# Performance work log

Hardware: AMD Instinct MI355X
Metric: run time of the kernel (lower is better)

## Reference

```python
import jax, jax.numpy as jnp
import numpy as np

SCALE = 1.0  # alpha / rank = 32 / 32


def setup_inputs() -> dict:
    key = jax.random.key(0)
    k_x, k_w, k_b, k_a, k_bb = jax.random.split(key, 5)
    B, S, D = 4, 4096, 3072
    depth, rank = 4, 32
    x = jax.random.normal(k_x, (B, S, D), dtype=jnp.float32)
    W = jax.random.normal(k_w, (D, D), dtype=jnp.float32) * (1.0 / np.sqrt(D))
    b = jax.random.normal(k_b, (D,), dtype=jnp.float32) * 0.02
    lora_A = jax.random.normal(k_a, (depth, rank, D), dtype=jnp.float32) * (1.0 / np.sqrt(D))
    lora_B = jax.random.normal(k_bb, (depth, D, rank), dtype=jnp.float32) * 0.02
    return {"x": x, "W": W, "b": b, "lora_A": lora_A, "lora_B": lora_B}


def reference(x, W, b, lora_A, lora_B):
    # base: y = x @ W.T + b
    base_out = jnp.einsum('bsi,oi->bso', x, W) + b
    # stacked LoRA: sum_d (x @ A_d.T @ B_d.T); dropout=0 -> identity
    # down-project to rank per depth: [B,S,depth,rank]
    z = jnp.einsum('bsi,dri->bsdr', x, lora_A)
    lora_out = jnp.einsum('bsdr,dor->bso', z, lora_B)
    return base_out + lora_out * SCALE
```

## Files before the change

### kernel.cpp

```cpp
#include <hip/hip_runtime.h>
#include <hip/hip_bf16.h>


typedef unsigned short ushort_t;
typedef short bf16x8 __attribute__((ext_vector_type(8)));
typedef float floatx4 __attribute__((ext_vector_type(4)));
typedef unsigned short ushortx4 __attribute__((ext_vector_type(4)));
typedef unsigned short ushortx8 __attribute__((ext_vector_type(8)));

__device__ __forceinline__ ushort_t f2bf(float f) {
    __hip_bfloat16 h = __float2bfloat16(f);
    return *(ushort_t*)&h;
}

__device__ __forceinline__ void async_load16(const void* g, void* l) {
    __builtin_amdgcn_global_load_lds(
        (const __attribute__((address_space(1))) void*)g,
        (__attribute__((address_space(3))) void*)l,
        16, 0, 0);
}

#define MFMA16(a, b, c) __builtin_amdgcn_mfma_f32_16x16x32_bf16(a, b, c, 0, 0, 0)

__global__ __launch_bounds__(256)
void cvt_kernel(const float* __restrict__ in, ushort_t* __restrict__ out, int n8) {
    int i = blockIdx.x * 256 + threadIdx.x;
    if (i < n8) {
        const float4 v0 = ((const float4*)in)[2 * i];
        const float4 v1 = ((const float4*)in)[2 * i + 1];
        ushortx8 o = { f2bf(v0.x), f2bf(v0.y), f2bf(v0.z), f2bf(v0.w),
                       f2bf(v1.x), f2bf(v1.y), f2bf(v1.z), f2bf(v1.w) };
        ((ushortx8*)out)[i] = o;
    }
}

__global__ __launch_bounds__(256)
void transpose_lora_kernel(const float* __restrict__ lb,
                           const float* __restrict__ la,
                           ushort_t* __restrict__ outB,
                           ushort_t* __restrict__ outA) {
    int bid = blockIdx.x;
    if (bid < 1536) {
        int idx = bid * 256 + threadIdx.x;
        int n = idx >> 7;
        int j = idx & 127;
        int d = j >> 5, r = j & 31;
        outB[idx] = f2bf(lb[(size_t)d * (3072 * 32) + (size_t)n * 32 + r]);
    } else {
        int idx = (bid - 1536) * 256 + threadIdx.x;
        int kk = idx >> 7;
        int j  = idx & 127;
        outA[idx] = f2bf(la[(size_t)j * 3072 + kk]);
    }
}

template <int KT, bool OUT_F32, bool ADD_MAT>
__global__ __launch_bounds__(256)
void gemm_bt_kernel(const ushort_t* __restrict__ A, int lda,
                    const ushort_t* __restrict__ B, int ldb,
                    const float* __restrict__ Cadd,
                    const float* __restrict__ bias,
                    void* __restrict__ Cv, int ldc)
{
    __shared__ ushort_t As[128 * 32];
    __shared__ ushort_t Bs[128 * 32];

    const int t    = threadIdx.x;
    const int lane = t & 63;
    const int wave = t >> 6;
    const int wr   = wave >> 1, wc = wave & 1;
    const int quad = lane >> 4, l16 = lane & 15;

    const int mBase = blockIdx.y * 128;
    const int nBase = blockIdx.x * 128;

    floatx4 acc[4][4] = {};

    const int p0 = t,       r0 = p0 >> 2, g0 = ((p0 & 3) ^ ((r0 >> 1) & 3)) << 3;
    const int p1 = t + 256, r1 = p1 >> 2, g1 = ((p1 & 3) ^ ((r1 >> 1) & 3)) << 3;
    const int qs = (quad ^ ((l16 >> 1) & 3)) << 3;

    for (int kt = 0; kt < KT; ++kt) {
        const int ko = kt * 32;

        async_load16(A + (size_t)(mBase + r0) * lda + ko + g0, &As[p0 * 8]);
        async_load16(A + (size_t)(mBase + r1) * lda + ko + g1, &As[p1 * 8]);
        async_load16(B + (size_t)(nBase + r0) * ldb + ko + g0, &Bs[p0 * 8]);
        async_load16(B + (size_t)(nBase + r1) * ldb + ko + g1, &Bs[p1 * 8]);

        __syncthreads();

        bf16x8 af[4], bf[4];
#pragma unroll
        for (int mi = 0; mi < 4; ++mi)
            af[mi] = *(const bf16x8*)&As[(wr * 64 + mi * 16 + l16) * 32 + qs];
#pragma unroll
        for (int ni = 0; ni < 4; ++ni)
            bf[ni] = *(const bf16x8*)&Bs[(wc * 64 + ni * 16 + l16) * 32 + qs];

#pragma unroll
        for (int mi = 0; mi < 4; ++mi)
#pragma unroll
            for (int ni = 0; ni < 4; ++ni)
                acc[mi][ni] = MFMA16(af[mi], bf[ni], acc[mi][ni]);

        __syncthreads();
    }

#pragma unroll
    for (int ni = 0; ni < 4; ++ni) {
        const int col = nBase + wc * 64 + ni * 16 + l16;
        const float bv = bias ? bias[col] : 0.0f;
#pragma unroll
        for (int mi = 0; mi < 4; ++mi) {
            const int row = mBase + wr * 64 + mi * 16 + quad * 4;
#pragma unroll
            for (int r = 0; r < 4; ++r) {
                float v = acc[mi][ni][r] + bv;
                if (ADD_MAT) v += Cadd[(size_t)(row + r) * ldc + col];
                if (OUT_F32) {
                    ((float*)Cv)[(size_t)(row + r) * ldc + col] = v;
                } else {
                    ((ushort_t*)Cv)[(size_t)(row + r) * ldc + col] = f2bf(v);
                }
            }
        }
    }
}

__global__ __launch_bounds__(512)
void gemm256_kernel(const ushort_t* __restrict__ A,
                    const ushort_t* __restrict__ B,
                    const float* __restrict__ bias,
                    float* __restrict__ C)
{
    constexpr int LDA = 3072;
    constexpr int NT  = 48;
    constexpr int NBX = 12;

    __shared__ ushort_t smem_u[81920];
    char* const smem = (char*)smem_u;

    const int t    = threadIdx.x;
    const int lane = t & 63;
    const int wave = t >> 6;
    const int wr   = wave >> 2;
    const int wc   = wave & 3;
    const int quad = lane >> 4;
    const int l16  = lane & 15;

    const int bid = blockIdx.x;
    const int sw  = (bid & 7) * 96 + (bid >> 3);
    const int bx  = sw % NBX;
    const int by  = sw / NBX;
    const int mBase = by * 256;
    const int nBase = bx * 256;

    const int prow = t >> 3;
    const int cg   = (t & 7) ^ (prow & 7);
    const ushort_t* const aSrc = A + (size_t)(mBase + prow) * LDA + cg * 8;
    const ushort_t* const bSrc = B + (size_t)(nBase + prow) * LDA + cg * 8;

#define STAGE_A(off, h, ktv) do {                                           \
        const ushort_t* _s = aSrc + (size_t)(h) * 128 * LDA + (ktv) * 64;   \
        char* _d = smem + (off) + (h) * 16384 + t * 16;                     \
        async_load16(_s, _d);                                               \
        async_load16(_s + 64 * LDA, _d + 8192);                             \
    } while (0)
#define STAGE_B(off, h, ktv) do {                                           \
        const ushort_t* _s = bSrc + (size_t)(h) * 128 * LDA + (ktv) * 64;   \
        char* _d = smem + (off) + (h) * 16384 + t * 16;                     \
        async_load16(_s, _d);                                               \
        async_load16(_s + 64 * LDA, _d + 8192);                             \
    } while (0)

    const int s0  = ((0 + quad) ^ (l16 & 7)) << 4;
    const int s1  = ((4 + quad) ^ (l16 & 7)) << 4;
    const int aRdB = wr * 16384 + l16 * 128;
    const int bRdB = (wc >> 1) * 16384 + ((wc & 1) * 64 + l16) * 128;

    floatx4 acc[8][4] = {};
    bf16x8 af[8][2];
    bf16x8 bfr[2][2];

    STAGE_A(0,      0, 0); STAGE_A(0,      1, 0);
    STAGE_B(65536,  0, 0); STAGE_B(65536,  1, 0);
    STAGE_A(32768,  0, 1); STAGE_A(32768,  1, 1);
    STAGE_B(98304,  0, 1); STAGE_B(98304,  1, 1);
    asm volatile("s_waitcnt vmcnt(8)" ::: "memory");
    __builtin_amdgcn_s_barrier();
    __builtin_amdgcn_sched_barrier(0);

    int aOff = 0;
    int bRdO = 65536;
    int bStO = 131072;

    for (int kt = 0; kt < NT; ++kt) {
        const int ktN = (kt + 2 < NT) ? kt + 2 : NT - 1;

#pragma unroll
        for (int mi = 0; mi < 4; ++mi) {
            af[mi][0] = *(const bf16x8*)(smem + aOff + aRdB + mi * 2048 + s0);
            af[mi][1] = *(const bf16x8*)(smem + aOff + aRdB + mi * 2048 + s1);
        }
#pragma unroll
        for (int nj = 0; nj < 2; ++nj) {
            bfr[nj][0] = *(const bf16x8*)(smem + bRdO + bRdB + nj * 2048 + s0);
            bfr[nj][1] = *(const bf16x8*)(smem + bRdO + bRdB + nj * 2048 + s1);
        }
        STAGE_B(bStO, 0, ktN);
        __builtin_amdgcn_s_barrier();
        asm volatile("s_waitcnt lgkmcnt(0)" ::: "memory");
        __builtin_amdgcn_sched_barrier(0);
        __builtin_amdgcn_s_setprio(1);
#pragma unroll
        for (int ks = 0; ks < 2; ++ks)
#pragma unroll
            for (int mi = 0; mi < 4; ++mi)
#pragma unroll
                for (int nj = 0; nj < 2; ++nj)
                    acc[mi][nj] = MFMA16(af[mi][ks], bfr[nj][ks], acc[mi][nj]);
        __builtin_amdgcn_s_setprio(0);
        __builtin_amdgcn_s_barrier();

#pragma unroll
        for (int mi = 4; mi < 8; ++mi) {
            af[mi][0] = *(const bf16x8*)(smem + aOff + aRdB + mi * 2048 + s0);
            af[mi][1] = *(const bf16x8*)(smem + aOff + aRdB + mi * 2048 + s1);
        }
        STAGE_B(bStO, 1, ktN);
        __builtin_amdgcn_s_barrier();
        asm volatile("s_waitcnt lgkmcnt(0)" ::: "memory");
        __builtin_amdgcn_sched_barrier(0);
        __builtin_amdgcn_s_setprio(1);
#pragma unroll
        for (int ks = 0; ks < 2; ++ks)
#pragma unroll
            for (int mi = 4; mi < 8; ++mi)
#pragma unroll
                for (int nj = 0; nj < 2; ++nj)
                    acc[mi][nj] = MFMA16(af[mi][ks], bfr[nj][ks], acc[mi][nj]);
        __builtin_amdgcn_s_setprio(0);
        __builtin_amdgcn_s_barrier();

#pragma unroll
        for (int nj = 0; nj < 2; ++nj) {
            bfr[nj][0] = *(const bf16x8*)(smem + bRdO + bRdB + (2 + nj) * 2048 + s0);
            bfr[nj][1] = *(const bf16x8*)(smem + bRdO + bRdB + (2 + nj) * 2048 + s1);
        }
        STAGE_A(aOff, 0, ktN);
        __builtin_amdgcn_s_barrier();
        asm volatile("s_waitcnt lgkmcnt(0)" ::: "memory");
        __builtin_amdgcn_sched_barrier(0);
        __builtin_amdgcn_s_setprio(1);
#pragma unroll
        for (int ks = 0; ks < 2; ++ks)
#pragma unroll
            for (int mi = 0; mi < 4; ++mi)
#pragma unroll
                for (int nj = 0; nj < 2; ++nj)
                    acc[mi][2 + nj] = MFMA16(af[mi][ks], bfr[nj][ks], acc[mi][2 + nj]);
        __builtin_amdgcn_s_setprio(0);
        __builtin_amdgcn_s_barrier();

        STAGE_A(aOff, 1, ktN);
        asm volatile("s_waitcnt vmcnt(8)" ::: "memory");
        __builtin_amdgcn_s_barrier();
        __builtin_amdgcn_sched_barrier(0);
        __builtin_amdgcn_s_setprio(1);
#pragma unroll
        for (int ks = 0; ks < 2; ++ks)
#pragma unroll
            for (int mi = 4; mi < 8; ++mi)
#pragma unroll
                for (int nj = 0; nj < 2; ++nj)
                    acc[mi][2 + nj] = MFMA16(af[mi][ks], bfr[nj][ks], acc[mi][2 + nj]);
        __builtin_amdgcn_s_setprio(0);
        __builtin_amdgcn_s_barrier();

        aOff ^= 32768;
        bRdO = (bRdO == 131072) ? 65536 : bRdO + 32768;
        bStO = (bStO == 131072) ? 65536 : bStO + 32768;
    }

    asm volatile("s_waitcnt vmcnt(0)" ::: "memory");

#pragma unroll
    for (int ni = 0; ni < 4; ++ni) {
        const int col = nBase + wc * 64 + ni * 16 + l16;
        const float bv = bias[col];
#pragma unroll
        for (int mi = 0; mi < 8; ++mi) {
            const int row0 = mBase + wr * 128 + mi * 16 + quad * 4;
            float* cp = C + (size_t)row0 * LDA + col;
#pragma unroll
            for (int r = 0; r < 4; ++r)
                cp[(size_t)r * LDA] = acc[mi][ni][r] + bv;
        }
    }
#undef STAGE_A
#undef STAGE_B
}

extern "C" void kernel_launch(void* const* d_in, const int* in_sizes, int n_in,
                              void* d_out, int out_size, void* d_ws, size_t ws_size,
                              hipStream_t stream) {
    const float* x  = (const float*)d_in[0];
    const float* W  = (const float*)d_in[1];
    const float* b  = (const float*)d_in[2];
    const float* lA = (const float*)d_in[3];
    const float* lB = (const float*)d_in[4];
    float* out = (float*)d_out;

    constexpr int M = 4 * 4096;
    constexpr int N = 3072;
    constexpr int K = 3072;
    constexpr size_t nX  = (size_t)M * K;
    constexpr size_t nW  = (size_t)N * K;
    constexpr size_t nT  = (size_t)128 * K;

    ushort_t* xb    = (ushort_t*)d_ws;
    ushort_t* Weffb = xb + nX;
    ushort_t* Bp    = Weffb + nW;
    ushort_t* At    = Bp + nT;

    cvt_kernel<<<nX / 8 / 256, 256, 0, stream>>>(x, xb, (int)(nX / 8));

    transpose_lora_kernel<<<2 * (nT / 256), 256, 0, stream>>>(lB, lA, Bp, At);

    gemm_bt_kernel<4, false, true><<<dim3(N / 128, N / 128), 256, 0, stream>>>(
        Bp, 128, At, 128, W, nullptr, Weffb, N);

    gemm256_kernel<<<(M / 256) * (N / 256), 512, 0, stream>>>(xb, Weffb, b, out);
}
```

Baseline: 633.4 us.

## Restructure GEMM k-loop into two phases with all fragments loaded upfront

Replaces the four-phase k-iteration, which interleaved partial LDS fragment loads, staging and barriers, with two phases. All A and B fragments for the tile are read from LDS at the start, then MFMAs for the first two column blocks are issued before a single barrier. After that barrier, the A staging is issued and the second half of the MFMAs runs. This cuts the number of barriers and waitcnt stalls per iteration. In exchange it holds more fragment registers live, and the first MFMAs can start without an explicit lgkmcnt wait on the fragment reads, leaving that ordering to the compiler.

After: 630.7 us. No clear change (-0.4%).

```diff
diff --git a/kernel.cpp b/kernel.cpp
--- a/kernel.cpp
+++ b/kernel.cpp
@@ -181,7 +181,7 @@
 
     floatx4 acc[8][4] = {};
     bf16x8 af[8][2];
-    bf16x8 bfr[2][2];
+    bf16x8 bfr[4][2];
 
     STAGE_A(0,      0, 0); STAGE_A(0,      1, 0);
     STAGE_B(65536,  0, 0); STAGE_B(65536,  1, 0);
@@ -198,85 +198,50 @@
     for (int kt = 0; kt < NT; ++kt) {
         const int ktN = (kt + 2 < NT) ? kt + 2 : NT - 1;
 
-#pragma unroll
-        for (int mi = 0; mi < 4; ++mi) {
+        STAGE_B(bStO, 0, ktN);
+        STAGE_B(bStO, 1, ktN);
+        __builtin_amdgcn_sched_barrier(0);
+
+#pragma unroll
+        for (int mi = 0; mi < 8; ++mi) {
             af[mi][0] = *(const bf16x8*)(smem + aOff + aRdB + mi * 2048 + s0);
             af[mi][1] = *(const bf16x8*)(smem + aOff + aRdB + mi * 2048 + s1);
         }
 #pragma unroll
-        for (int nj = 0; nj < 2; ++nj) {
+        for (int nj = 0; nj < 4; ++nj) {
             bfr[nj][0] = *(const bf16x8*)(smem + bRdO + bRdB + nj * 2048 + s0);
             bfr[nj][1] = *(const bf16x8*)(smem + bRdO + bRdB + nj * 2048 + s1);
         }
-        STAGE_B(bStO, 0, ktN);
-        __builtin_amdgcn_s_barrier();
-        asm volatile("s_waitcnt lgkmcnt(0)" ::: "memory");
-        __builtin_amdgcn_sched_barrier(0);
-        __builtin_amdgcn_s_setprio(1);
 #pragma unroll
         for (int ks = 0; ks < 2; ++ks)
 #pragma unroll
-            for (int mi = 0; mi < 4; ++mi)
+            for (int mi = 0; mi < 8; ++mi)
 #pragma unroll
                 for (int nj = 0; nj < 2; ++nj)
                     acc[mi][nj] = MFMA16(af[mi][ks], bfr[nj][ks], acc[mi][nj]);
+
+        asm volatile("s_waitcnt lgkmcnt(0)" ::: "memory");
+        __builtin_amdgcn_sched_barrier(0);
+        __builtin_amdgcn_s_barrier();
+
+        STAGE_A(aOff, 0, ktN);
+        STAGE_A(aOff, 1, ktN);
+        __builtin_amdgcn_sched_barrier(0);
+
+        __builtin_amdgcn_s_setprio(1);
+#pragma unroll
+        for (int ks = 0; ks < 2; ++ks)
+#pragma unroll
+            for (int mi = 0; mi < 8; ++mi)
+#pragma unroll
+                for (int nj = 0; nj < 2; ++nj)
+                    acc[mi][2 + nj] = MFMA16(af[mi][ks], bfr[2 + nj][ks],
+                                             acc[mi][2 + nj]);
         __builtin_amdgcn_s_setprio(0);
-        __builtin_amdgcn_s_barrier();
-
-#pragma unroll
-        for (int mi = 4; mi < 8; ++mi) {
-            af[mi][0] = *(const bf16x8*)(smem + aOff + aRdB + mi * 2048 + s0);
-            af[mi][1] = *(const bf16x8*)(smem + aOff + aRdB + mi * 2048 + s1);
-        }
-        STAGE_B(bStO, 1, ktN);
-        __builtin_amdgcn_s_barrier();
-        asm volatile("s_waitcnt lgkmcnt(0)" ::: "memory");
-        __builtin_amdgcn_sched_barrier(0);
-        __builtin_amdgcn_s_setprio(1);
-#pragma unroll
-        for (int ks = 0; ks < 2; ++ks)
-#pragma unroll
-            for (int mi = 4; mi < 8; ++mi)
-#pragma unroll
-                for (int nj = 0; nj < 2; ++nj)
-                    acc[mi][nj] = MFMA16(af[mi][ks], bfr[nj][ks], acc[mi][nj]);
-        __builtin_amdgcn_s_setprio(0);
-        __builtin_amdgcn_s_barrier();
-
-#pragma unroll
-        for (int nj = 0; nj < 2; ++nj) {
-            bfr[nj][0] = *(const bf16x8*)(smem + bRdO + bRdB + (2 + nj) * 2048 + s0);
-            bfr[nj][1] = *(const bf16x8*)(smem + bRdO + bRdB + (2 + nj) * 2048 + s1);
-        }
-        STAGE_A(aOff, 0, ktN);
-        __builtin_amdgcn_s_barrier();
-        asm volatile("s_waitcnt lgkmcnt(0)" ::: "memory");
-        __builtin_amdgcn_sched_barrier(0);
-        __builtin_amdgcn_s_setprio(1);
-#pragma unroll
-        for (int ks = 0; ks < 2; ++ks)
-#pragma unroll
-            for (int mi = 0; mi < 4; ++mi)
-#pragma unroll
-                for (int nj = 0; nj < 2; ++nj)
-                    acc[mi][2 + nj] = MFMA16(af[mi][ks], bfr[nj][ks], acc[mi][2 + nj]);
-        __builtin_amdgcn_s_setprio(0);
-        __builtin_amdgcn_s_barrier();
-
-        STAGE_A(aOff, 1, ktN);
+        __builtin_amdgcn_sched_barrier(0);
         asm volatile("s_waitcnt vmcnt(8)" ::: "memory");
         __builtin_amdgcn_s_barrier();
         __builtin_amdgcn_sched_barrier(0);
-        __builtin_amdgcn_s_setprio(1);
-#pragma unroll
-        for (int ks = 0; ks < 2; ++ks)
-#pragma unroll
-            for (int mi = 4; mi < 8; ++mi)
-#pragma unroll
-                for (int nj = 0; nj < 2; ++nj)
-                    acc[mi][2 + nj] = MFMA16(af[mi][ks], bfr[nj][ks], acc[mi][2 + nj]);
-        __builtin_amdgcn_s_setprio(0);
-        __builtin_amdgcn_s_barrier();
 
         aOff ^= 32768;
         bRdO = (bRdO == 131072) ? 65536 : bRdO + 32768;
```
